# Performance work log

Hardware: AMD Instinct MI355X
Metric: run time of the kernel (lower is better)

The kernel has to match this reference:

```python
import jax, jax.numpy as jnp
import numpy as np

M, K, N = 8192, 4096, 4096  # tokens, in_features, out_features
QMAX = 127.0


def setup_inputs() -> dict:
    key = jax.random.key(0)
    kx, kw, ks, kb = jax.random.split(key, 4)
    x = jax.random.normal(kx, (M, K), dtype=jnp.float32)
    # Build w_q / s_w the same way from_float would: per-output-channel symmetric quant
    w = jax.random.normal(kw, (N, K), dtype=jnp.float32) * 0.02
    s_w = (jnp.max(jnp.abs(w), axis=1, keepdims=True) / QMAX).astype(jnp.float32)  # [N,1]
    w_q = jnp.clip(jnp.round(w / s_w), -QMAX, QMAX).astype(jnp.int8)  # [N,K] int8
    bias = jax.random.normal(kb, (N,), dtype=jnp.float32) * 0.01
    return {"x": x, "w_q": w_q, "s_w": s_w, "bias": bias}


def reference(x, w_q, s_w, bias):
    # mode == 'W8A8_dynamic': per-tensor symmetric activation quant (zp = 0)
    s_x = jnp.max(jnp.abs(x)) / QMAX                       # scalar scale
    x_q = jnp.clip(jnp.round(x / s_x), -QMAX, QMAX)        # int8 values held in fp32
    # fake-dequant matmul: (x_q @ w_q^T) * (s_x * s_w^T) + bias
    y_int = x_q @ w_q.astype(jnp.float32).T                # [M, N]
    y = y_int * (s_x * s_w.astype(jnp.float32).T)          # broadcast [1,N]
    y = y + bias
    return y.astype(x.dtype)
```

## Files before the change

kernel.cpp:

```cpp
#include <hip/hip_runtime.h>
#include <stdint.h>

#define QMAXF 127.0f

constexpr int Mdim = 8192;
constexpr int Kdim = 4096;
constexpr int Ndim = 4096;
constexpr int PREP_BLOCKS = 2048;

using i32x4 = __attribute__((ext_vector_type(4))) int;

__device__ __forceinline__ void async_copy16(const void* g, void* l) {
    __builtin_amdgcn_global_load_lds(
        (const __attribute__((address_space(1))) void*)g,
        (__attribute__((address_space(3))) void*)l,
        16, 0, 0);
}

__global__ void prep_kernel(const float* __restrict__ x,
                            const int* __restrict__ w32,
                            float* __restrict__ blockmax,
                            int8_t* __restrict__ w8) {
    float m = 0.f;
    const float4* x4 = (const float4*)x;
    const int n4x = Mdim * Kdim / 4;
    for (int i = blockIdx.x * blockDim.x + threadIdx.x; i < n4x;
         i += gridDim.x * blockDim.x) {
        float4 v = x4[i];
        m = fmaxf(fmaxf(fabsf(v.x), fabsf(v.y)),
                  fmaxf(m, fmaxf(fabsf(v.z), fabsf(v.w))));
    }
#pragma unroll
    for (int off = 32; off > 0; off >>= 1)
        m = fmaxf(m, __shfl_down(m, off, 64));
    __shared__ float red[4];
    if ((threadIdx.x & 63) == 0) red[threadIdx.x >> 6] = m;
    __syncthreads();
    if (threadIdx.x == 0)
        blockmax[blockIdx.x] =
            fmaxf(fmaxf(red[0], red[1]), fmaxf(red[2], red[3]));

    const int4* in4 = (const int4*)w32;
    char4* out4 = (char4*)w8;
    const int n4w = Ndim * Kdim / 4;
    for (int i = blockIdx.x * blockDim.x + threadIdx.x; i < n4w;
         i += gridDim.x * blockDim.x) {
        int4 v = in4[i];
        char4 c;
        c.x = (signed char)v.x;
        c.y = (signed char)v.y;
        c.z = (signed char)v.z;
        c.w = (signed char)v.w;
        out4[i] = c;
    }
}

__global__ void finalize_kernel(const float* __restrict__ blockmax,
                                float* __restrict__ sx) {
    float m = 0.f;
    for (int i = threadIdx.x; i < PREP_BLOCKS; i += 256)
        m = fmaxf(m, blockmax[i]);
#pragma unroll
    for (int off = 32; off > 0; off >>= 1)
        m = fmaxf(m, __shfl_down(m, off, 64));
    __shared__ float red[4];
    if ((threadIdx.x & 63) == 0) red[threadIdx.x >> 6] = m;
    __syncthreads();
    if (threadIdx.x == 0)
        *sx = fmaxf(fmaxf(red[0], red[1]), fmaxf(red[2], red[3])) / QMAXF;
}

__global__ void quant_x_kernel(const float* __restrict__ x,
                               const float* __restrict__ sxp,
                               int8_t* __restrict__ xq, int n4) {
    const float s = *sxp;
    const float4* x4 = (const float4*)x;
    char4* q4 = (char4*)xq;
    for (int i = blockIdx.x * blockDim.x + threadIdx.x; i < n4;
         i += gridDim.x * blockDim.x) {
        float4 v = x4[i];
        char4 q;
        q.x = (signed char)(int)fminf(QMAXF, fmaxf(-QMAXF, rintf(v.x / s)));
        q.y = (signed char)(int)fminf(QMAXF, fmaxf(-QMAXF, rintf(v.y / s)));
        q.z = (signed char)(int)fminf(QMAXF, fmaxf(-QMAXF, rintf(v.z / s)));
        q.w = (signed char)(int)fminf(QMAXF, fmaxf(-QMAXF, rintf(v.w / s)));
        q4[i] = q;
    }
}

#define BM 128
#define BN 128
#define BK 128

__global__ __launch_bounds__(256) void gemm_i8_kernel(
    const int8_t* __restrict__ Xq, const int8_t* __restrict__ Wq,
    const float* __restrict__ sxp, const float* __restrict__ s_w,
    const float* __restrict__ bias, float* __restrict__ Y) {
    __shared__ int8_t As[BM * BK];
    __shared__ int8_t Bs[BN * BK];

    const int t = threadIdx.x;
    const int w = t >> 6;
    const int l = t & 63;
    const int lane15 = l & 15;
    const int lquad = l >> 4;
    const int swz = lane15 & 7;
    const int wm = (w >> 1) * 64;
    const int wn = (w & 1) * 64;

    const int bm = blockIdx.y * BM;
    const int bn = blockIdx.x * BN;

    const int8_t* aptr[4];
    const int8_t* bptr[4];
#pragma unroll
    for (int s = 0; s < 4; s++) {
        const int cl = t + 256 * s;
        const int r = cl >> 3;
        const int c = ((cl & 7) ^ (r & 7)) * 16;
        aptr[s] = Xq + (size_t)(bm + r) * Kdim + c;
        bptr[s] = Wq + (size_t)(bn + r) * Kdim + c;
    }
    int8_t* alds[4];
    int8_t* blds[4];
#pragma unroll
    for (int s = 0; s < 4; s++) {
        alds[s] = As + s * 4096 + w * 1024;
        blds[s] = Bs + s * 4096 + w * 1024;
    }

    i32x4 acc[4][4] = {};

    for (int kt = 0; kt < Kdim; kt += BK) {
#pragma unroll
        for (int s = 0; s < 4; s++) async_copy16(aptr[s] + kt, alds[s]);
#pragma unroll
        for (int s = 0; s < 4; s++) async_copy16(bptr[s] + kt, blds[s]);
        __syncthreads();

#pragma unroll
        for (int kk = 0; kk < 2; kk++) {
            i32x4 a[4], b[4];
#pragma unroll
            for (int i = 0; i < 4; i++)
                a[i] = *(const i32x4*)(As + (wm + i * 16 + lane15) * BK +
                                       (((kk << 2) | lquad) ^ swz) * 16);
#pragma unroll
            for (int j = 0; j < 4; j++)
                b[j] = *(const i32x4*)(Bs + (wn + j * 16 + lane15) * BK +
                                       (((kk << 2) | lquad) ^ swz) * 16);
#pragma unroll
            for (int i = 0; i < 4; i++)
#pragma unroll
                for (int j = 0; j < 4; j++)
                    acc[i][j] = __builtin_amdgcn_mfma_i32_16x16x64_i8(
                        a[i], b[j], acc[i][j], 0, 0, 0);
        }
        __syncthreads();
    }

    const float sx = *sxp;
#pragma unroll
    for (int j = 0; j < 4; j++) {
        const int col = bn + wn + j * 16 + lane15;
        const float sc = sx * s_w[col];
        const float bs = bias[col];
#pragma unroll
        for (int i = 0; i < 4; i++) {
            const int row = bm + wm + i * 16 + lquad * 4;
            float* yp = Y + (size_t)row * Ndim + col;
#pragma unroll
            for (int r = 0; r < 4; r++)
                yp[(size_t)r * Ndim] = (float)acc[i][j][r] * sc + bs;
        }
    }
}

extern "C" void kernel_launch(void* const* d_in, const int* in_sizes, int n_in,
                              void* d_out, int out_size, void* d_ws,
                              size_t ws_size, hipStream_t stream) {
    const float* x = (const float*)d_in[0];
    const int* w_q = (const int*)d_in[1];
    const float* s_w = (const float*)d_in[2];
    const float* bias = (const float*)d_in[3];
    float* y = (float*)d_out;

    float* sx = (float*)d_ws;
    float* blockmax = (float*)((char*)d_ws + 256);
    int8_t* xq = (int8_t*)d_ws + 16384;
    int8_t* wq8 = (int8_t*)d_ws + 16384 + (size_t)Mdim * Kdim;

    prep_kernel<<<PREP_BLOCKS, 256, 0, stream>>>(x, w_q, blockmax, wq8);
    finalize_kernel<<<1, 256, 0, stream>>>(blockmax, sx);
    quant_x_kernel<<<PREP_BLOCKS, 256, 0, stream>>>(x, sx, xq,
                                                    Mdim * Kdim / 4);

    dim3 grid(Ndim / BN, Mdim / BM);
    gemm_i8_kernel<<<grid, 256, 0, stream>>>(xq, wq8, sx, s_w, bias, y);
}
```

Baseline: 434.1 us.

## Rewrite int8 GEMM with 256x256 tiles, double-buffered LDS and interleaved MFMA quadrants

The int8 GEMM now uses 256x256 block tiles with 512 threads and a 128KB double-buffered LDS. Global-to-LDS async copies for the next k-tiles are interleaved with four MFMA quadrant phases, using explicit waitcnt and barriers and raised wave priority during MFMA. Blocks are remapped with a grid swizzle for better L2 reuse. This aims to hide load latency and raise arithmetic intensity per block, at the cost of higher register and LDS pressure and a fragile hand-tuned wait schedule.

```diff
diff --git a/kernel.cpp b/kernel.cpp
--- a/kernel.cpp
+++ b/kernel.cpp
@@ -88,90 +88,162 @@
     }
 }
 
-#define BM 128
-#define BN 128
-#define BK 128
-
-__global__ __launch_bounds__(256) void gemm_i8_kernel(
+#define BM 256
+#define BN 256
+#define BKB 128
+#define NKT (Kdim / BKB)
+
+#define BAR() __builtin_amdgcn_s_barrier()
+#define LGKM0()                                           \
+    do {                                                  \
+        asm volatile("s_waitcnt lgkmcnt(0)" ::: "memory");\
+        __builtin_amdgcn_sched_barrier(0);                \
+    } while (0)
+
+__global__ __launch_bounds__(512, 2) void gemm_i8_kernel(
     const int8_t* __restrict__ Xq, const int8_t* __restrict__ Wq,
     const float* __restrict__ sxp, const float* __restrict__ s_w,
     const float* __restrict__ bias, float* __restrict__ Y) {
-    __shared__ int8_t As[BM * BK];
-    __shared__ int8_t Bs[BN * BK];
+    __shared__ int8_t lds[131072];
 
     const int t = threadIdx.x;
     const int w = t >> 6;
     const int l = t & 63;
     const int lane15 = l & 15;
     const int lquad = l >> 4;
-    const int swz = lane15 & 7;
-    const int wm = (w >> 1) * 64;
-    const int wn = (w & 1) * 64;
-
-    const int bm = blockIdx.y * BM;
-    const int bn = blockIdx.x * BN;
-
-    const int8_t* aptr[4];
-    const int8_t* bptr[4];
-#pragma unroll
-    for (int s = 0; s < 4; s++) {
-        const int cl = t + 256 * s;
-        const int r = cl >> 3;
-        const int c = ((cl & 7) ^ (r & 7)) * 16;
-        aptr[s] = Xq + (size_t)(bm + r) * Kdim + c;
-        bptr[s] = Wq + (size_t)(bn + r) * Kdim + c;
-    }
-    int8_t* alds[4];
-    int8_t* blds[4];
-#pragma unroll
-    for (int s = 0; s < 4; s++) {
-        alds[s] = As + s * 4096 + w * 1024;
-        blds[s] = Bs + s * 4096 + w * 1024;
-    }
-
-    i32x4 acc[4][4] = {};
-
-    for (int kt = 0; kt < Kdim; kt += BK) {
-#pragma unroll
-        for (int s = 0; s < 4; s++) async_copy16(aptr[s] + kt, alds[s]);
-#pragma unroll
-        for (int s = 0; s < 4; s++) async_copy16(bptr[s] + kt, blds[s]);
-        __syncthreads();
-
-#pragma unroll
-        for (int kk = 0; kk < 2; kk++) {
-            i32x4 a[4], b[4];
-#pragma unroll
-            for (int i = 0; i < 4; i++)
-                a[i] = *(const i32x4*)(As + (wm + i * 16 + lane15) * BK +
-                                       (((kk << 2) | lquad) ^ swz) * 16);
-#pragma unroll
-            for (int j = 0; j < 4; j++)
-                b[j] = *(const i32x4*)(Bs + (wn + j * 16 + lane15) * BK +
-                                       (((kk << 2) | lquad) ^ swz) * 16);
-#pragma unroll
-            for (int i = 0; i < 4; i++)
-#pragma unroll
-                for (int j = 0; j < 4; j++)
-                    acc[i][j] = __builtin_amdgcn_mfma_i32_16x16x64_i8(
-                        a[i], b[j], acc[i][j], 0, 0, 0);
-        }
-        __syncthreads();
+    const int swz7 = l & 7;
+
+    const int flat = blockIdx.y * gridDim.x + blockIdx.x;
+    const int swzb = (flat & 7) * 64 + (flat >> 3);
+    const int bn = (swzb & 15) * BN;
+    const int bm = (swzb >> 4) * BM;
+
+    const int r0 = t >> 3;
+    const int cOff = ((t & 7) ^ (r0 & 7)) * 16;
+    const int8_t* aS = Xq + (size_t)(bm + r0) * Kdim + cOff;
+    const int8_t* bS = Wq + (size_t)(bn + r0) * Kdim + cOff;
+    const int wb = w * 1024;
+
+    const int aRdBase = ((w >> 2) * 64 + lane15) * BKB;
+    const int bRdBase = ((w & 3) * 32 + lane15) * BKB;
+    const int kOff0 = (lquad ^ swz7) * 16;
+    const int kOff1 = kOff0 ^ 64;
+
+    i32x4 acc[2][2][4][2] = {};
+    i32x4 a[4][2], b[2][2];
+
+    int8_t* const ldsA_ = lds;
+    int8_t* const ldsB_ = lds + 32768;
+
+#define STAGE(SRC, LBASE, h, kt)                                              \
+    do {                                                                      \
+        if ((kt) < NKT) {                                                     \
+            const int8_t* _s =                                                \
+                (SRC) + (size_t)(h) * 128 * Kdim + (size_t)(kt) * BKB;        \
+            int8_t* _d = (LBASE) + ((kt) & 1) * 65536 + (h) * 16384 + wb;     \
+            async_copy16(_s, _d);                                             \
+            async_copy16(_s + (size_t)64 * Kdim, _d + 8192);                  \
+        }                                                                     \
+    } while (0)
+
+#define LDA(mh)                                                               \
+    {                                                                         \
+        _Pragma("unroll") for (int i = 0; i < 4; ++i) {                       \
+            a[i][0] = *(const i32x4*)(curA + aRdBase + (mh) * 16384 +         \
+                                      i * 2048 + kOff0);                      \
+            a[i][1] = *(const i32x4*)(curA + aRdBase + (mh) * 16384 +         \
+                                      i * 2048 + kOff1);                      \
+        }                                                                     \
+    }
+
+#define LDB(nh)                                                               \
+    {                                                                         \
+        _Pragma("unroll") for (int j = 0; j < 2; ++j) {                       \
+            b[j][0] = *(const i32x4*)(curB + bRdBase + (nh) * 16384 +         \
+                                      j * 2048 + kOff0);                      \
+            b[j][1] = *(const i32x4*)(curB + bRdBase + (nh) * 16384 +         \
+                                      j * 2048 + kOff1);                      \
+        }                                                                     \
+    }
+
+#define MFMA_Q(mh, nh)                                                        \
+    do {                                                                      \
+        __builtin_amdgcn_s_setprio(1);                                        \
+        _Pragma("unroll") for (int i = 0; i < 4; ++i)                         \
+            _Pragma("unroll") for (int j = 0; j < 2; ++j) {                   \
+            acc[mh][nh][i][j] = __builtin_amdgcn_mfma_i32_16x16x64_i8(        \
+                a[i][0], b[j][0], acc[mh][nh][i][j], 0, 0, 0);                \
+            acc[mh][nh][i][j] = __builtin_amdgcn_mfma_i32_16x16x64_i8(        \
+                a[i][1], b[j][1], acc[mh][nh][i][j], 0, 0, 0);                \
+        }                                                                     \
+        __builtin_amdgcn_s_setprio(0);                                        \
+    } while (0)
+
+#define GROUP(T, BOFF)                                                        \
+    do {                                                                      \
+        const int8_t* curA = ldsA_ + (BOFF);                                  \
+        const int8_t* curB = ldsB_ + (BOFF);                                  \
+                                                                      \
+        LDA(0); LDB(0);                                                       \
+        STAGE(bS, ldsB_, 0, (T) + 1);                                         \
+        asm volatile("s_waitcnt lgkmcnt(8)" ::: "memory");                    \
+        BAR(); LGKM0(); MFMA_Q(0, 0); BAR();                                  \
+                                                                      \
+        LDB(1);                                                               \
+        STAGE(aS, ldsA_, 0, (T) + 2);                                         \
+        BAR(); LGKM0(); MFMA_Q(0, 1); BAR();                                  \
+                                                                      \
+        LDA(1);                                                               \
+        STAGE(bS, ldsB_, 1, (T) + 2);                                         \
+        BAR(); LGKM0(); MFMA_Q(1, 1); BAR();                                  \
+                                                                      \
+        LDB(0);                                                               \
+        STAGE(aS, ldsA_, 1, (T) + 2);                                         \
+        if ((T) + 2 < NKT) {                                                  \
+            asm volatile("s_waitcnt vmcnt(6)" ::: "memory");                  \
+        } else {                                                              \
+            asm volatile("s_waitcnt vmcnt(0)" ::: "memory");                  \
+        }                                                                     \
+        BAR(); LGKM0(); MFMA_Q(1, 0); BAR();                                  \
+    } while (0)
+
+    STAGE(aS, ldsA_, 0, 0);
+    STAGE(bS, ldsB_, 1, 0);
+    STAGE(aS, ldsA_, 1, 0);
+    STAGE(bS, ldsB_, 0, 0);
+    STAGE(aS, ldsA_, 0, 1);
+    STAGE(bS, ldsB_, 1, 1);
+    STAGE(aS, ldsA_, 1, 1);
+    asm volatile("s_waitcnt vmcnt(6)" ::: "memory");
+    BAR();
+
+    for (int t2 = 0; t2 < NKT; t2 += 2) {
+        GROUP(t2, 0);
+        GROUP(t2 + 1, 65536);
     }
 
     const float sx = *sxp;
-#pragma unroll
-    for (int j = 0; j < 4; j++) {
-        const int col = bn + wn + j * 16 + lane15;
-        const float sc = sx * s_w[col];
-        const float bs = bias[col];
-#pragma unroll
-        for (int i = 0; i < 4; i++) {
-            const int row = bm + wm + i * 16 + lquad * 4;
-            float* yp = Y + (size_t)row * Ndim + col;
-#pragma unroll
-            for (int r = 0; r < 4; r++)
-                yp[(size_t)r * Ndim] = (float)acc[i][j][r] * sc + bs;
+    const int wmE = (w >> 2) * 64;
+    const int wnE = (w & 3) * 32;
+#pragma unroll
+    for (int nh = 0; nh < 2; ++nh) {
+#pragma unroll
+        for (int j = 0; j < 2; ++j) {
+            const int col = bn + nh * 128 + wnE + j * 16 + lane15;
+            const float sc = sx * s_w[col];
+            const float bs = bias[col];
+#pragma unroll
+            for (int mh = 0; mh < 2; ++mh) {
+#pragma unroll
+                for (int i = 0; i < 4; ++i) {
+                    const int row = bm + mh * 128 + wmE + i * 16 + lquad * 4;
+                    float* yp = Y + (size_t)row * Ndim + col;
+#pragma unroll
+                    for (int r = 0; r < 4; ++r)
+                        yp[(size_t)r * Ndim] =
+                            (float)acc[mh][nh][i][j][r] * sc + bs;
+                }
+            }
         }
     }
 }
@@ -196,5 +268,5 @@
                                                     Mdim * Kdim / 4);
 
     dim3 grid(Ndim / BN, Mdim / BM);
-    gemm_i8_kernel<<<grid, 256, 0, stream>>>(xq, wq8, sx, s_w, bias, y);
-}
+    gemm_i8_kernel<<<grid, 512, 0, stream>>>(xq, wq8, sx, s_w, bias, y);
+}
```

Result: faster. 411.5 us (-5.2%).
